# Kernel optimization log

Measured on AMD Instinct MI355X. Metric: run time of the kernel, lower is better.

## Reference

```python
import jax, jax.numpy as jnp
import numpy as np

DN = ('NCH', 'OIH', 'NCH')  # conv dimension numbers: [batch, channel, length]

def setup_inputs() -> dict:
    key = jax.random.key(0)
    ks = jax.random.split(key, 8)
    B, S, L, D, F, V = 16, 64, 128, 512, 256, 30000
    return {
        'text': jax.random.randint(ks[0], (B, S, L), 0, V),
        'embed': jax.random.normal(ks[1], (V, D), dtype=jnp.float32),
        'w3': jax.random.normal(ks[2], (F, D, 3), dtype=jnp.float32) * 0.05,
        'b3': jax.random.normal(ks[3], (F,), dtype=jnp.float32) * 0.05,
        'w4': jax.random.normal(ks[4], (F, D, 4), dtype=jnp.float32) * 0.05,
        'b4': jax.random.normal(ks[5], (F,), dtype=jnp.float32) * 0.05,
        'w5': jax.random.normal(ks[6], (F, D, 5), dtype=jnp.float32) * 0.05,
        'b5': jax.random.normal(ks[7], (F,), dtype=jnp.float32) * 0.05,
    }

def reference(text, embed, w3, b3, w4, b4, w5, b5):
    B, S, L = text.shape
    # Embed tokens, flatten episodes x utterances into one batch, channels-first.
    x = embed[text]                                   # [B, S, L, D]
    x = x.reshape(B * S, L, -1).transpose(0, 2, 1)    # [BS, D, L]
    outs = []
    for w, b in ((w3, b3), (w4, b4), (w5, b5)):
        y = jax.lax.conv_general_dilated(x, w, (1,), 'VALID', dimension_numbers=DN)
        # max-over-time pooling (valid conv -> length L-K+1)
        outs.append(jnp.max(y + b[None, :, None], axis=2))  # [BS, F]
    out = jax.nn.relu(jnp.concatenate(outs, axis=1))  # [BS, 3F]
    return out.reshape(B, S, -1)
```

## Files before the change

kernel.cpp:

```cpp
#include <hip/hip_runtime.h>
#include <hip/hip_bf16.h>


typedef __bf16 bf16x8 __attribute__((ext_vector_type(8)));
typedef float f32x4 __attribute__((ext_vector_type(4)));

#define ROWS 132
#define ROWB 512
#define BUF_BYTES (ROWS * ROWB)
#define RED_OFF (2 * BUF_BYTES)
#define LDS_TOTAL (2 * BUF_BYTES + 2048)
#define WQ_ELEMS 1572864

__global__ void pack_w_kernel(const float* __restrict__ w3,
                              const float* __restrict__ w4,
                              const float* __restrict__ w5,
                              __bf16* __restrict__ wq) {
    const int t    = blockIdx.x * 256 + threadIdx.x;
    const int g    = t >> 6;
    const int lane = t & 63;
    int rel, Kw; const float* w;
    if (g < 768)       { rel = g;        Kw = 3; w = w3; }
    else if (g < 1792) { rel = g - 768;  Kw = 4; w = w4; }
    else               { rel = g - 1792; Kw = 5; w = w5; }
    const int kq  = rel >> 4;
    const int n16 = rel & 15;
    const int f   = n16 * 16 + (lane & 15);
    const int k0  = kq * 32 + (lane >> 4) * 8;
    const int tap = k0 >> 9;
    const int d0  = k0 & 511;
    const float* src = w + ((size_t)f * 512 + d0) * Kw + tap;
    bf16x8 o;
#pragma unroll
    for (int j = 0; j < 8; ++j) o[j] = (__bf16)src[j * Kw];
    *(bf16x8*)(wq + (size_t)t * 8) = o;
}

__global__ __launch_bounds__(1024, 4) void conv_gemm_kernel(
        const int* __restrict__ text,
        const float* __restrict__ embed,
        const __bf16* __restrict__ wq,
        const float* __restrict__ b3,
        const float* __restrict__ b4,
        const float* __restrict__ b5,
        float* __restrict__ out) {
    extern __shared__ char lds[];
    char* const buf0 = lds;
    char* const buf1 = lds + BUF_BYTES;
    float* const red = (float*)(lds + RED_OFF);

    const int tid  = threadIdx.x;
    const int lane = tid & 63;
    const int wave = tid >> 6;
    const int wm = wave & 1;
    const int wn = wave >> 1;
    const int lm = lane & 15, lk = lane >> 4;
    const int sr = tid >> 5;
    const int sc = tid & 31;

    float4 G[4];
    auto issuePair = [&](int nbs, int h, int p0) {
#pragma unroll
        for (int p = 0; p < 2; ++p) {
            const int r = (p0 + p) * 32 + sr;
            const int tok = text[nbs * 128 + r];
            const float* src = embed + (size_t)tok * 512 + h * 256 + sc * 8;
            G[p * 2]     = *(const float4*)(src);
            G[p * 2 + 1] = *(const float4*)(src + 4);
        }
    };
    auto writePair = [&](char* bufp, int p0) {
#pragma unroll
        for (int p = 0; p < 2; ++p) {
            const int r = (p0 + p) * 32 + sr;
            const float4 v0 = G[p * 2], v1 = G[p * 2 + 1];
            bf16x8 o;
            o[0] = (__bf16)v0.x; o[1] = (__bf16)v0.y;
            o[2] = (__bf16)v0.z; o[3] = (__bf16)v0.w;
            o[4] = (__bf16)v1.x; o[5] = (__bf16)v1.y;
            o[6] = (__bf16)v1.z; o[7] = (__bf16)v1.w;
            *(bf16x8*)(bufp + r * ROWB + ((sc * 16) ^ ((r & 7) << 4))) = o;
        }
    };

    f32x4 acc[4][2];
    bf16x8 B4[4][2];
    const __bf16* bp = wq;

    auto loadB = [&](bf16x8* d, int kb) {
        const __bf16* p = bp + (size_t)kb * 8192;
        d[0] = *(const bf16x8*)(p);
        d[1] = *(const bf16x8*)(p + 512);
    };

    auto runPhase = [&](const char* bufp, int KW, int h) {
        const int kh = h * 8;
        const int maxkq = (KW - 1) * 16 + kh + 7;
        loadB(B4[0], kh);     loadB(B4[1], kh + 1);
        loadB(B4[2], kh + 2); loadB(B4[3], kh + 3);
        for (int tap = 0; tap < KW; ++tap) {
            int P[4][2];
#pragma unroll
            for (int mt = 0; mt < 4; ++mt) {
                const int row = wm * 64 + mt * 16 + lm + tap;
                const int x46 = (row & 7) << 4;
                const int Bb  = row * ROWB + ((lk * 16) ^ (x46 & 48));
                const int E   = x46 & 64;
                P[mt][0] = Bb + E;
                P[mt][1] = Bb + 64 - E;
            }
            const int kqt = tap * 16 + kh;
#pragma unroll
            for (int q = 0; q < 8; ++q) {
                bf16x8 a[4];
#pragma unroll
                for (int mt = 0; mt < 4; ++mt)
                    a[mt] = *(const bf16x8*)(bufp + P[mt][q & 1] + (q >> 1) * 128);
                __builtin_amdgcn_s_setprio(1);
#pragma unroll
                for (int nt = 0; nt < 2; ++nt)
#pragma unroll
                    for (int mt = 0; mt < 4; ++mt)
                        acc[mt][nt] = __builtin_amdgcn_mfma_f32_16x16x32_bf16(
                            a[mt], B4[q & 3][nt], acc[mt][nt], 0, 0, 0);
                __builtin_amdgcn_s_setprio(0);
                int kqn = kqt + ((q < 4) ? (q + 4) : (q + 12));
                kqn = (kqn <= maxkq) ? kqn : maxkq;
                loadB(B4[q & 3], kqn);
            }
        }
    };

    const int bsbase = blockIdx.x * 4;
    issuePair(bsbase, 0, 0); writePair(buf0, 0);
    issuePair(bsbase, 0, 2); writePair(buf0, 2);
    issuePair(bsbase, 1, 0); writePair(buf1, 0);
    issuePair(bsbase, 1, 2); writePair(buf1, 2);
    if (tid < 128) {
        const int r = 128 + sr;
        const int off = r * ROWB + ((sc * 16) ^ ((r & 7) << 4));
        bf16x8 z = {};
        *(bf16x8*)(buf0 + off) = z;
        *(bf16x8*)(buf1 + off) = z;
    }
    __syncthreads();

#pragma unroll 1
    for (int i = 0; i < 4; ++i) {
        const int bs  = bsbase + i;
        const int nbs = bs + 1;
        const bool stg = (i < 3);
#pragma unroll 1
        for (int c = 0; c < 3; ++c) {
            const int KW = 3 + c;
            bp = wq + ((c == 0) ? 0 : (c == 1) ? 393216 : 917504)
                    + (size_t)wn * 1024 + (size_t)lane * 8;
#pragma unroll
            for (int mt = 0; mt < 4; ++mt)
#pragma unroll
                for (int nt = 0; nt < 2; ++nt)
                    acc[mt][nt] = (f32x4){0.f, 0.f, 0.f, 0.f};

            const bool lastc = stg && (c == 2);
            if (lastc) issuePair(nbs, 0, 0);
            runPhase(buf0, KW, 0);
            if (lastc) {
                __syncthreads();
                writePair(buf0, 0);
                issuePair(nbs, 0, 2);
                writePair(buf0, 2);
                issuePair(nbs, 1, 0);
            }
            runPhase(buf1, KW, 1);

            const int Tv = 126 - c;
            float cmax[2];
#pragma unroll
            for (int nt = 0; nt < 2; ++nt) {
                float mx = -3.0e38f;
#pragma unroll
                for (int mt = 0; mt < 4; ++mt) {
                    const int mb = wm * 64 + mt * 16 + lk * 4;
#pragma unroll
                    for (int r = 0; r < 4; ++r)
                        if (mb + r < Tv) mx = fmaxf(mx, acc[mt][nt][r]);
                }
                mx = fmaxf(mx, __shfl_xor(mx, 16, 64));
                mx = fmaxf(mx, __shfl_xor(mx, 32, 64));
                cmax[nt] = mx;
            }
            __syncthreads();
            if (lastc) {
                writePair(buf1, 0);
                issuePair(nbs, 1, 2);
                writePair(buf1, 2);
            }
            if (lk == 0) {
#pragma unroll
                for (int nt = 0; nt < 2; ++nt)
                    red[wm * 256 + wn * 32 + nt * 16 + lm] = cmax[nt];
            }
            __syncthreads();
            if (tid < 256) {
                const float* bias = (c == 0) ? b3 : (c == 1) ? b4 : b5;
                const float v = fmaxf(red[tid], red[256 + tid]) + bias[tid];
                out[(size_t)bs * 768 + c * 256 + tid] = fmaxf(v, 0.f);
            }
        }
    }
}

extern "C" void kernel_launch(void* const* d_in, const int* in_sizes, int n_in,
                              void* d_out, int out_size, void* d_ws, size_t ws_size,
                              hipStream_t stream) {
    const int*   text  = (const int*)d_in[0];
    const float* embed = (const float*)d_in[1];
    const float* w3    = (const float*)d_in[2];
    const float* b3    = (const float*)d_in[3];
    const float* w4    = (const float*)d_in[4];
    const float* b4    = (const float*)d_in[5];
    const float* w5    = (const float*)d_in[6];
    const float* b5    = (const float*)d_in[7];
    float* out = (float*)d_out;

    __bf16* wq = (__bf16*)d_ws;

    (void)hipFuncSetAttribute((const void*)conv_gemm_kernel,
                              hipFuncAttributeMaxDynamicSharedMemorySize,
                              LDS_TOTAL);

    pack_w_kernel<<<768, 256, 0, stream>>>(w3, w4, w5, wq);
    conv_gemm_kernel<<<256, 1024, LDS_TOTAL, stream>>>(text, embed, wq,
                                                       b3, b4, b5, out);
}
```

Measured before the change: 441.7 us.

## Switch conv GEMM to 32x32x16 MFMA with 4x4 wave tiling

Replaces the 16x16x32 bf16 MFMA tiling (2 M-waves x 8 N-waves, 4x2 tiles per wave) with 32x32x16 MFMA on a 4x4 wave grid, each wave holding two 32x32 accumulators. The packed weight layout, the LDS swizzle, the A-operand software prefetch (one-step lookahead including across taps and halves) and the B register pipeline, which now prefetches across conv widths, are all rewritten to match. The reduction scratch grows to four M-slices. The aim is fewer MFMA issues and better operand reuse per LDS read, at the cost of more complex index logic and more accumulator registers.

```diff
diff --git a/kernel.cpp b/kernel.cpp
--- a/kernel.cpp
+++ b/kernel.cpp
@@ -4,12 +4,13 @@
 
 typedef __bf16 bf16x8 __attribute__((ext_vector_type(8)));
 typedef float f32x4 __attribute__((ext_vector_type(4)));
+typedef float f32x16 __attribute__((ext_vector_type(16)));
 
 #define ROWS 132
 #define ROWB 512
 #define BUF_BYTES (ROWS * ROWB)
 #define RED_OFF (2 * BUF_BYTES)
-#define LDS_TOTAL (2 * BUF_BYTES + 2048)
+#define LDS_TOTAL (RED_OFF + 4096)
 #define WQ_ELEMS 1572864
 
 __global__ void pack_w_kernel(const float* __restrict__ w3,
@@ -23,12 +24,11 @@
     if (g < 768)       { rel = g;        Kw = 3; w = w3; }
     else if (g < 1792) { rel = g - 768;  Kw = 4; w = w4; }
     else               { rel = g - 1792; Kw = 5; w = w5; }
-    const int kq  = rel >> 4;
-    const int n16 = rel & 15;
-    const int f   = n16 * 16 + (lane & 15);
-    const int k0  = kq * 32 + (lane >> 4) * 8;
-    const int tap = k0 >> 9;
-    const int d0  = k0 & 511;
+    const int k16 = rel >> 3;
+    const int n32 = rel & 7;
+    const int f   = n32 * 32 + (lane & 31);
+    const int tap = k16 >> 5;
+    const int d0  = (k16 & 31) * 16 + (lane >> 5) * 8;
     const float* src = w + ((size_t)f * 512 + d0) * Kw + tap;
     bf16x8 o;
 #pragma unroll
@@ -45,18 +45,19 @@
         const float* __restrict__ b5,
         float* __restrict__ out) {
     extern __shared__ char lds[];
-    char* const buf0 = lds;
-    char* const buf1 = lds + BUF_BYTES;
     float* const red = (float*)(lds + RED_OFF);
 
     const int tid  = threadIdx.x;
     const int lane = tid & 63;
     const int wave = tid >> 6;
-    const int wm = wave & 1;
-    const int wn = wave >> 1;
-    const int lm = lane & 15, lk = lane >> 4;
-    const int sr = tid >> 5;
-    const int sc = tid & 31;
+    const int wm   = wave & 3;
+    const int wn   = wave >> 2;
+    const int l31  = lane & 31;
+    const int lh   = lane >> 5;
+    const int sr   = tid >> 5;
+    const int sc   = tid & 31;
+
+    const int bsbase = blockIdx.x * 4;
 
     float4 G[4];
     auto issuePair = [&](int nbs, int h, int p0) {
@@ -79,69 +80,29 @@
             o[2] = (__bf16)v0.z; o[3] = (__bf16)v0.w;
             o[4] = (__bf16)v1.x; o[5] = (__bf16)v1.y;
             o[6] = (__bf16)v1.z; o[7] = (__bf16)v1.w;
-            *(bf16x8*)(bufp + r * ROWB + ((sc * 16) ^ ((r & 7) << 4))) = o;
+            *(bf16x8*)(bufp + r * ROWB + (((sc ^ (r & 7))) << 4)) = o;
         }
     };
 
-    f32x4 acc[4][2];
-    bf16x8 B4[4][2];
-    const __bf16* bp = wq;
-
-    auto loadB = [&](bf16x8* d, int kb) {
-        const __bf16* p = bp + (size_t)kb * 8192;
-        d[0] = *(const bf16x8*)(p);
-        d[1] = *(const bf16x8*)(p + 512);
-    };
-
-    auto runPhase = [&](const char* bufp, int KW, int h) {
-        const int kh = h * 8;
-        const int maxkq = (KW - 1) * 16 + kh + 7;
-        loadB(B4[0], kh);     loadB(B4[1], kh + 1);
-        loadB(B4[2], kh + 2); loadB(B4[3], kh + 3);
-        for (int tap = 0; tap < KW; ++tap) {
-            int P[4][2];
-#pragma unroll
-            for (int mt = 0; mt < 4; ++mt) {
-                const int row = wm * 64 + mt * 16 + lm + tap;
-                const int x46 = (row & 7) << 4;
-                const int Bb  = row * ROWB + ((lk * 16) ^ (x46 & 48));
-                const int E   = x46 & 64;
-                P[mt][0] = Bb + E;
-                P[mt][1] = Bb + 64 - E;
-            }
-            const int kqt = tap * 16 + kh;
-#pragma unroll
-            for (int q = 0; q < 8; ++q) {
-                bf16x8 a[4];
-#pragma unroll
-                for (int mt = 0; mt < 4; ++mt)
-                    a[mt] = *(const bf16x8*)(bufp + P[mt][q & 1] + (q >> 1) * 128);
-                __builtin_amdgcn_s_setprio(1);
-#pragma unroll
-                for (int nt = 0; nt < 2; ++nt)
-#pragma unroll
-                    for (int mt = 0; mt < 4; ++mt)
-                        acc[mt][nt] = __builtin_amdgcn_mfma_f32_16x16x32_bf16(
-                            a[mt], B4[q & 3][nt], acc[mt][nt], 0, 0, 0);
-                __builtin_amdgcn_s_setprio(0);
-                int kqn = kqt + ((q < 4) ? (q + 4) : (q + 12));
-                kqn = (kqn <= maxkq) ? kqn : maxkq;
-                loadB(B4[q & 3], kqn);
-            }
-        }
-    };
-
-    const int bsbase = blockIdx.x * 4;
-    issuePair(bsbase, 0, 0); writePair(buf0, 0);
-    issuePair(bsbase, 0, 2); writePair(buf0, 2);
-    issuePair(bsbase, 1, 0); writePair(buf1, 0);
-    issuePair(bsbase, 1, 2); writePair(buf1, 2);
+    f32x16 acc[2];
+    bf16x8 Br[4][2];
+    const __bf16* const bpL = wq + (size_t)wn * 1024 + (size_t)lane * 8;
+
+    issuePair(bsbase, 0, 0); writePair(lds, 0);
+    issuePair(bsbase, 0, 2); writePair(lds, 2);
+    issuePair(bsbase, 1, 0); writePair(lds + BUF_BYTES, 0);
+    issuePair(bsbase, 1, 2); writePair(lds + BUF_BYTES, 2);
     if (tid < 128) {
         const int r = 128 + sr;
-        const int off = r * ROWB + ((sc * 16) ^ ((r & 7) << 4));
+        const int off = r * ROWB + ((sc ^ (r & 7)) << 4);
         bf16x8 z = {};
-        *(bf16x8*)(buf0 + off) = z;
-        *(bf16x8*)(buf1 + off) = z;
+        *(bf16x8*)(lds + off) = z;
+        *(bf16x8*)(lds + BUF_BYTES + off) = z;
+    }
+#pragma unroll
+    for (int k = 0; k < 4; ++k) {
+        Br[k][0] = *(const bf16x8*)(bpL + k * 4096);
+        Br[k][1] = *(const bf16x8*)(bpL + k * 4096 + 512);
     }
     __syncthreads();
 
@@ -153,25 +114,72 @@
 #pragma unroll 1
         for (int c = 0; c < 3; ++c) {
             const int KW = 3 + c;
-            bp = wq + ((c == 0) ? 0 : (c == 1) ? 393216 : 917504)
-                    + (size_t)wn * 1024 + (size_t)lane * 8;
-#pragma unroll
-            for (int mt = 0; mt < 4; ++mt)
-#pragma unroll
-                for (int nt = 0; nt < 2; ++nt)
-                    acc[mt][nt] = (f32x4){0.f, 0.f, 0.f, 0.f};
-
+            const size_t cb  = (c == 0) ? 0 : (c == 1) ? 393216 : 917504;
+            const size_t cbn = (c == 2) ? 0 : (c == 0) ? 393216 : 917504;
+            const __bf16* bpc = bpL + cb;
+            const __bf16* bpn = bpL + cbn;
             const bool lastc = stg && (c == 2);
+#pragma unroll
+            for (int r = 0; r < 16; ++r) { acc[0][r] = 0.f; acc[1][r] = 0.f; }
+
             if (lastc) issuePair(nbs, 0, 0);
-            runPhase(buf0, KW, 0);
-            if (lastc) {
-                __syncthreads();
-                writePair(buf0, 0);
-                issuePair(nbs, 0, 2);
-                writePair(buf0, 2);
-                issuePair(nbs, 1, 0);
-            }
-            runPhase(buf1, KW, 1);
+
+            const int arow = wm * 32 + l31;
+            bf16x8 a_cur = *(const bf16x8*)(
+                lds + arow * 512 + ((lh ^ (arow & 7)) << 4));
+
+#pragma unroll 1
+            for (int h = 0; h < 2; ++h) {
+                const int hb = h * 16;
+                const int bo = h ? BUF_BYTES : 0;
+#pragma unroll 1
+                for (int tap = 0; tap < KW; ++tap) {
+                    const int row = arow + tap;
+                    const int v   = row & 7;
+                    const int rb  = bo + row * 512;
+                    int P[4];
+#pragma unroll
+                    for (int k = 0; k < 4; ++k)
+                        P[k] = rb + (((k * 2 + lh) ^ v) << 4);
+                    int R0;
+                    if (tap < KW - 1) {
+                        const int r2 = row + 1;
+                        R0 = bo + r2 * 512 + ((lh ^ (r2 & 7)) << 4);
+                    } else if (h == 0) {
+                        R0 = BUF_BYTES + arow * 512 + ((lh ^ (arow & 7)) << 4);
+                    } else R0 = P[0];
+                    const int t1 = tap * 32 + hb + 4;
+                    int t2; bool pn = false;
+                    if (tap < KW - 1)  t2 = tap * 32 + hb + 20;
+                    else if (h == 0)   t2 = 4;
+                    else             { t2 = -12; pn = true; }
+#pragma unroll
+                    for (int s = 0; s < 16; ++s) {
+                        const bf16x8 a_n = *(const bf16x8*)(lds +
+                            ((s < 15) ? P[(s + 1) & 3] + (((s + 1) >> 2) << 7)
+                                      : R0));
+                        __builtin_amdgcn_s_setprio(1);
+                        acc[0] = __builtin_amdgcn_mfma_f32_32x32x16_bf16(
+                            a_cur, Br[s & 3][0], acc[0], 0, 0, 0);
+                        acc[1] = __builtin_amdgcn_mfma_f32_32x32x16_bf16(
+                            a_cur, Br[s & 3][1], acc[1], 0, 0, 0);
+                        __builtin_amdgcn_s_setprio(0);
+                        const int tk = (s < 12) ? (t1 + s) : (t2 + s);
+                        const __bf16* p =
+                            (((s >= 12) && pn) ? bpn : bpc) + (size_t)tk * 4096;
+                        Br[s & 3][0] = *(const bf16x8*)(p);
+                        Br[s & 3][1] = *(const bf16x8*)(p + 512);
+                        a_cur = a_n;
+                    }
+                }
+                if (h == 0 && lastc) {
+                    __syncthreads();
+                    writePair(lds, 0);
+                    issuePair(nbs, 0, 2);
+                    writePair(lds, 2);
+                    issuePair(nbs, 1, 0);
+                }
+            }
 
             const int Tv = 126 - c;
             float cmax[2];
@@ -179,32 +187,30 @@
             for (int nt = 0; nt < 2; ++nt) {
                 float mx = -3.0e38f;
 #pragma unroll
-                for (int mt = 0; mt < 4; ++mt) {
-                    const int mb = wm * 64 + mt * 16 + lk * 4;
-#pragma unroll
-                    for (int r = 0; r < 4; ++r)
-                        if (mb + r < Tv) mx = fmaxf(mx, acc[mt][nt][r]);
+                for (int r = 0; r < 16; ++r) {
+                    const int t = wm * 32 + (r & 3) + 8 * (r >> 2) + 4 * lh;
+                    if (t < Tv) mx = fmaxf(mx, acc[nt][r]);
                 }
-                mx = fmaxf(mx, __shfl_xor(mx, 16, 64));
                 mx = fmaxf(mx, __shfl_xor(mx, 32, 64));
                 cmax[nt] = mx;
             }
             __syncthreads();
             if (lastc) {
-                writePair(buf1, 0);
+                writePair(lds + BUF_BYTES, 0);
                 issuePair(nbs, 1, 2);
-                writePair(buf1, 2);
-            }
-            if (lk == 0) {
-#pragma unroll
-                for (int nt = 0; nt < 2; ++nt)
-                    red[wm * 256 + wn * 32 + nt * 16 + lm] = cmax[nt];
+                writePair(lds + BUF_BYTES, 2);
+            }
+            if (lane < 32) {
+                red[wm * 256 + wn * 64 + l31]      = cmax[0];
+                red[wm * 256 + wn * 64 + 32 + l31] = cmax[1];
             }
             __syncthreads();
             if (tid < 256) {
                 const float* bias = (c == 0) ? b3 : (c == 1) ? b4 : b5;
-                const float v = fmaxf(red[tid], red[256 + tid]) + bias[tid];
-                out[(size_t)bs * 768 + c * 256 + tid] = fmaxf(v, 0.f);
+                const float vv = fmaxf(fmaxf(red[tid], red[256 + tid]),
+                                       fmaxf(red[512 + tid], red[768 + tid]))
+                                 + bias[tid];
+                out[(size_t)bs * 768 + c * 256 + tid] = fmaxf(vv, 0.f);
             }
         }
     }
```

After: 533.9 us. 1.21x slower.
